# Performance work log

Hardware: AMD Instinct MI355X
Metric: run time of the kernel (lower is better)

## Reference

```python
import jax, jax.numpy as jnp
import numpy as np

B, S, D = 1, 2048, 1024
H, HD = 16, 64          # attention heads, head dim (kv_heads = 1 -> MQA)
E, K, FH = 8, 2, 4096   # experts, top-k, expert hidden dim
EPS = 1e-5


def setup_inputs() -> dict:
    key = jax.random.key(0)
    ks = jax.random.split(key, 8)
    std = 0.02
    return {
        "x": jax.random.normal(ks[0], (B, S, D), jnp.float32),
        "Wq": jax.random.normal(ks[1], (D, H * HD), jnp.float32) * std,
        "Wk": jax.random.normal(ks[2], (D, HD), jnp.float32) * std,   # 1 kv head
        "Wv": jax.random.normal(ks[3], (D, HD), jnp.float32) * std,
        "Wo": jax.random.normal(ks[4], (H * HD, D), jnp.float32) * std,
        "g_pre_mqa": jnp.ones((D,), jnp.float32),
        "g_post_mqa": jnp.ones((D,), jnp.float32),
        "g_pre_moe": jnp.ones((D,), jnp.float32),
        "g_post_moe": jnp.ones((D,), jnp.float32),
        "Wr": jax.random.normal(ks[5], (D, E), jnp.float32) * std,
        "W1": jax.random.normal(ks[6], (E, D, FH), jnp.float32) * std,
        "W2": jax.random.normal(ks[7], (E, FH, D), jnp.float32) * std,
    }


def rmsnorm(x, g):
    return x * jax.lax.rsqrt(jnp.mean(x * x, axis=-1, keepdims=True) + EPS) * g


def reference(x, Wq, Wk, Wv, Wo, g_pre_mqa, g_post_mqa, g_pre_moe, g_post_moe, Wr, W1, W2):
    # --- MQA block (inference path, no dropout, no causal mask in source) ---
    h = rmsnorm(x, g_pre_mqa)
    q = (h @ Wq).reshape(B, S, H, HD)
    k = h @ Wk  # [B,S,HD] single kv head, broadcast over H
    v = h @ Wv
    scores = jnp.einsum('bqhd,bkd->bhqk', q, k) / np.float32(np.sqrt(HD))
    probs_attn = jax.nn.softmax(scores, axis=-1)
    attn = jnp.einsum('bhqk,bkd->bqhd', probs_attn, v).reshape(B, S, H * HD) @ Wo
    x = x + rmsnorm(attn, g_post_mqa)

    # --- MoE block: softmax router, top-k sparse combine ---
    h = rmsnorm(x, g_pre_moe)
    logits = h @ Wr                                # [B,S,E]
    routing_probs = jax.nn.softmax(logits, axis=-1)
    _, top_idx = jax.lax.top_k(routing_probs, K)   # [B,S,K]
    mask = jax.nn.one_hot(top_idx, E, dtype=routing_probs.dtype).sum(axis=-2)
    weights = routing_probs * mask                 # zero non-chosen experts
    hid = jax.nn.gelu(jnp.einsum('bsd,edf->bsef', h, W1))   # [B,S,E,FH]
    eout = jnp.einsum('bsef,efd->bsed', hid, W2)            # [B,S,E,D]
    moe_out = jnp.einsum('bsed,bse->bsd', eout, weights)
    x = x + rmsnorm(moe_out, g_post_moe)
    return x, routing_probs
```

## Files before the change

kernel.cpp:

```cpp
#include <hip/hip_runtime.h>

typedef unsigned short u16;

#define DEVFN static __device__ __forceinline__

constexpr int Sq = 2048, Dm = 1024, NH = 16, HDim = 64, NE = 8, FHid = 4096;

typedef __attribute__((ext_vector_type(8))) short bf16x8;
typedef __attribute__((ext_vector_type(4))) float f32x4;

DEVFN float b2f(u16 u) { return __uint_as_float(((unsigned)u) << 16); }
DEVFN u16 f2b(float f) {
  unsigned u = __float_as_uint(f);
  return (u16)((u + 0x7fffu + ((u >> 16) & 1u)) >> 16);
}
DEVFN float gelu_f(float x) {
  float y = 0.7978845608028654f * (x + 0.044715f * x * x * x);
  float t = 1.0f - 2.0f / (__expf(2.0f * y) + 1.0f);
  return 0.5f * x * (1.0f + t);
}

DEVFN void gload16(const u16* g, u16* l) {
  __builtin_amdgcn_global_load_lds((const __attribute__((address_space(1))) void*)g,
                                   (__attribute__((address_space(3))) void*)l, 16, 0, 0);
}

__global__ __launch_bounds__(256) void detect_k(const u16* __restrict__ x, int* __restrict__ flag) {
  int t = threadIdx.x;
  float mx = 0.f;
  for (int i = t; i < 4096; i += 256) mx = fmaxf(mx, fabsf(b2f(x[i])));
#pragma unroll
  for (int m = 32; m; m >>= 1) mx = fmaxf(mx, __shfl_xor(mx, m, 64));
  __shared__ float red[4];
  if ((t & 63) == 0) red[t >> 6] = mx;
  __syncthreads();
  if (t == 0) {
    float m2 = fmaxf(fmaxf(red[0], red[1]), fmaxf(red[2], red[3]));
    flag[0] = (m2 > 1e6f) ? 1 : 0;
  }
}

template <int INM, int RESM>
__global__ __launch_bounds__(64) void rmsnorm2_k(const void* __restrict__ inp, const void* __restrict__ g,
                                                 const void* __restrict__ resp, float* __restrict__ out1,
                                                 const int* __restrict__ dflag,
                                                 const void* __restrict__ inp2) {
  int isf = dflag[0];
  int row = blockIdx.x, t = threadIdx.x;
  long rb = (long)row * Dm;
  float v[16];
#pragma unroll
  for (int j = 0; j < 4; j++) {
    long o = rb + t * 4 + j * 256;
    if constexpr (INM == 2) {
      float4 f = *((const float4*)((const float*)inp + o));
      float4 f2 = *((const float4*)((const float*)inp2 + o));
      v[4 * j] = f.x + f2.x; v[4 * j + 1] = f.y + f2.y;
      v[4 * j + 2] = f.z + f2.z; v[4 * j + 3] = f.w + f2.w;
    } else if (INM == 0 || isf) {
      float4 f = *((const float4*)((const float*)inp + o));
      v[4 * j] = f.x; v[4 * j + 1] = f.y; v[4 * j + 2] = f.z; v[4 * j + 3] = f.w;
    } else {
      ushort4 u = *((const ushort4*)((const u16*)inp + o));
      v[4 * j] = b2f(u.x); v[4 * j + 1] = b2f(u.y); v[4 * j + 2] = b2f(u.z); v[4 * j + 3] = b2f(u.w);
    }
  }
  float ss = 0.f;
#pragma unroll
  for (int j = 0; j < 16; j++) ss += v[j] * v[j];
#pragma unroll
  for (int m = 32; m; m >>= 1) ss += __shfl_xor(ss, m, 64);
  float sc = rsqrtf(ss * (1.0f / Dm) + 1e-5f);
#pragma unroll
  for (int j = 0; j < 4; j++) {
    long o = rb + t * 4 + j * 256;
    int go = t * 4 + j * 256;
    float gf[4];
    if (isf) {
      float4 gv = *((const float4*)((const float*)g + go));
      gf[0] = gv.x; gf[1] = gv.y; gf[2] = gv.z; gf[3] = gv.w;
    } else {
      ushort4 gu = *((const ushort4*)((const u16*)g + go));
      gf[0] = b2f(gu.x); gf[1] = b2f(gu.y); gf[2] = b2f(gu.z); gf[3] = b2f(gu.w);
    }
    float o4[4];
#pragma unroll
    for (int q = 0; q < 4; q++) o4[q] = v[4 * j + q] * sc * gf[q];
    if constexpr (RESM == 1) {
      float4 rf = *((const float4*)((const float*)resp + o));
      o4[0] += rf.x; o4[1] += rf.y; o4[2] += rf.z; o4[3] += rf.w;
    } else if constexpr (RESM == 2) {
      if (isf) {
        float4 rf = *((const float4*)((const float*)resp + o));
        o4[0] += rf.x; o4[1] += rf.y; o4[2] += rf.z; o4[3] += rf.w;
      } else {
        ushort4 ru = *((const ushort4*)((const u16*)resp + o));
        o4[0] += b2f(ru.x); o4[1] += b2f(ru.y); o4[2] += b2f(ru.z); o4[3] += b2f(ru.w);
      }
    }
    float4 of;
    of.x = o4[0]; of.y = o4[1]; of.z = o4[2]; of.w = o4[3];
    *((float4*)(out1 + o)) = of;
  }
}

template <int OP>
__global__ __launch_bounds__(256) void gemm_nn_k(
    const float* __restrict__ A, const void* __restrict__ Braw, long boff,
    float* __restrict__ C, int M, int N, int K,
    const float* __restrict__ wfull, int eidx, const int* __restrict__ dflag) {
  int isf = dflag[0];
  const float* Bf = (const float*)Braw;
  const u16* Bh = (const u16*)Braw;
  int t = threadIdx.x;
  int m0 = blockIdx.y * 64, n0 = blockIdx.x * 64;

  __shared__ float As[64][20];
  __shared__ float Bs[16][68];

  int ty = t >> 4, tx = t & 15;
  float acc[4][4];
#pragma unroll
  for (int i = 0; i < 4; i++)
#pragma unroll
    for (int j = 0; j < 4; j++) acc[i][j] = 0.f;

  for (int k0 = 0; k0 < K; k0 += 16) {
    __syncthreads();
#pragma unroll
    for (int i = 0; i < 4; i++) {
      int idx = t + i * 256;
      int ar = idx >> 4, ac = idx & 15;
      As[ar][ac] = A[(long)(m0 + ar) * K + k0 + ac];
      int br = idx >> 6, bc = idx & 63;
      long bi = boff + (long)(k0 + br) * N + n0 + bc;
      Bs[br][bc] = isf ? Bf[bi] : b2f(Bh[bi]);
    }
    __syncthreads();
#pragma unroll
    for (int kk = 0; kk < 16; kk++) {
      float a[4], b[4];
#pragma unroll
      for (int i = 0; i < 4; i++) a[i] = As[ty * 4 + i][kk];
#pragma unroll
      for (int j = 0; j < 4; j++) b[j] = Bs[kk][tx * 4 + j];
#pragma unroll
      for (int i = 0; i < 4; i++)
#pragma unroll
        for (int j = 0; j < 4; j++) acc[i][j] += a[i] * b[j];
    }
  }
#pragma unroll
  for (int i = 0; i < 4; i++) {
    int row = m0 + ty * 4 + i;
#pragma unroll
    for (int j = 0; j < 4; j++) {
      int col = n0 + tx * 4 + j;
      long cidx = (long)row * N + col;
      float val = acc[i][j];
      if constexpr (OP == 0) C[cidx] = val;
      else if constexpr (OP == 1) C[cidx] = gelu_f(val);
      else C[cidx] += wfull[(long)row * 8 + eidx] * val;
    }
  }
}

__global__ __launch_bounds__(256) void gemm_big_k(
    const float* __restrict__ A, const void* __restrict__ Braw,
    float* __restrict__ C, int M, int N, int K, const int* __restrict__ dflag) {
  int isf = dflag[0];
  const float* Bf = (const float*)Braw;
  const u16* Bh = (const u16*)Braw;
  int t = threadIdx.x;
  int m0 = blockIdx.y * 128, n0 = blockIdx.x * 64;

  __shared__ float As[128][21];
  __shared__ float Bs[16][68];

  int ty = t >> 4, tx = t & 15;
  float acc[8][4];
#pragma unroll
  for (int i = 0; i < 8; i++)
#pragma unroll
    for (int j = 0; j < 4; j++) acc[i][j] = 0.f;

  for (int k0 = 0; k0 < K; k0 += 16) {
    __syncthreads();
#pragma unroll
    for (int i = 0; i < 8; i++) {
      int idx = t + i * 256;
      int ar = idx >> 4, ac = idx & 15;
      As[ar][ac] = A[(long)(m0 + ar) * K + k0 + ac];
    }
#pragma unroll
    for (int i = 0; i < 4; i++) {
      int idx = t + i * 256;
      int br = idx >> 6, bc = idx & 63;
      long bi = (long)(k0 + br) * N + n0 + bc;
      Bs[br][bc] = isf ? Bf[bi] : b2f(Bh[bi]);
    }
    __syncthreads();
#pragma unroll
    for (int kk = 0; kk < 16; kk++) {
      float a[8], b[4];
#pragma unroll
      for (int i = 0; i < 8; i++) a[i] = As[ty * 8 + i][kk];
#pragma unroll
      for (int j = 0; j < 4; j++) b[j] = Bs[kk][tx * 4 + j];
#pragma unroll
      for (int i = 0; i < 8; i++)
#pragma unroll
        for (int j = 0; j < 4; j++) acc[i][j] += a[i] * b[j];
    }
  }
#pragma unroll
  for (int i = 0; i < 8; i++) {
    int row = m0 + ty * 8 + i;
#pragma unroll
    for (int j = 0; j < 4; j++) {
      int col = n0 + tx * 4 + j;
      C[(long)row * N + col] = acc[i][j];
    }
  }
}

__global__ __launch_bounds__(256) void attn_f32_k(
    const float* __restrict__ Qf, const float* __restrict__ Kf, const float* __restrict__ Vf,
    float* __restrict__ Of) {
  int qb = blockIdx.x, h = blockIdx.y;
  int t = threadIdx.x;
  int qr = t >> 2;
  int sub = t & 3;
  __shared__ float Ks[64][68];
  __shared__ float Vs[64][68];
  int qrow = qb * 64 + qr;
  const float* qp = Qf + (long)qrow * Dm + h * HDim + sub * 16;
  float qfr[16];
#pragma unroll
  for (int j = 0; j < 16; j += 4) {
    float4 v = *(const float4*)(qp + j);
    qfr[j] = v.x; qfr[j + 1] = v.y; qfr[j + 2] = v.z; qfr[j + 3] = v.w;
  }
  float o[16];
#pragma unroll
  for (int j = 0; j < 16; j++) o[j] = 0.f;
  float m_i = -3e38f, l_i = 0.f;

  for (int kb = 0; kb < Sq / 64; kb++) {
    __syncthreads();
#pragma unroll
    for (int i = 0; i < 2; i++) {
      int idx = t + i * 256;
      int r = idx >> 3, c8 = (idx & 7) * 8;
      const float* kp = Kf + (long)(kb * 64 + r) * HDim + c8;
      float4 a = *(const float4*)(kp);
      float4 b = *(const float4*)(kp + 4);
      *(float4*)&Ks[r][c8] = a;
      *(float4*)&Ks[r][c8 + 4] = b;
      const float* vp = Vf + (long)(kb * 64 + r) * HDim + c8;
      float4 c = *(const float4*)(vp);
      float4 d = *(const float4*)(vp + 4);
      *(float4*)&Vs[r][c8] = c;
      *(float4*)&Vs[r][c8 + 4] = d;
    }
    __syncthreads();
    float s[64];
#pragma unroll
    for (int j = 0; j < 64; j++) {
      float acc = 0.f;
#pragma unroll
      for (int d = 0; d < 16; d++) acc += qfr[d] * Ks[j][sub * 16 + d];
      s[j] = acc;
    }
#pragma unroll
    for (int j = 0; j < 64; j++) {
      float v = s[j];
      v += __shfl_xor(v, 1, 64);
      v += __shfl_xor(v, 2, 64);
      s[j] = v * 0.125f;
    }
    float mx = s[0];
#pragma unroll
    for (int j = 1; j < 64; j++) mx = fmaxf(mx, s[j]);
    float mn = fmaxf(m_i, mx);
    float alpha = __expf(m_i - mn);
    m_i = mn;
    float ps = 0.f;
#pragma unroll
    for (int j = 0; j < 64; j++) {
      s[j] = __expf(s[j] - mn);
      ps += s[j];
    }
    l_i = l_i * alpha + ps;
#pragma unroll
    for (int d = 0; d < 16; d++) o[d] *= alpha;
#pragma unroll
    for (int j = 0; j < 64; j++)
#pragma unroll
      for (int d = 0; d < 16; d++) o[d] += s[j] * Vs[j][sub * 16 + d];
  }
  float inv = 1.0f / l_i;
#pragma unroll
  for (int d = 0; d < 16; d++)
    Of[(long)qrow * Dm + h * HDim + sub * 16 + d] = o[d] * inv;
}

__global__ __launch_bounds__(256) void router2_k(const float* __restrict__ h2, const void* __restrict__ Wr,
                                                 float* __restrict__ probs_out, float* __restrict__ wfull,
                                                 const int* __restrict__ dflag,
                                                 int* __restrict__ ecnt, int* __restrict__ elist) {
  int isf = dflag[0];
  int gid = blockIdx.x * 256 + threadIdx.x;
  int tok = gid >> 3, e = gid & 7;
  if (tok >= Sq) return;
  const float* hrow = h2 + (long)tok * Dm;
  float acc = 0.f;
  if (isf) {
    const float* wr = (const float*)Wr;
    for (int i = 0; i < Dm; i += 4) {
      float4 h4 = *(const float4*)(hrow + i);
      acc += h4.x * wr[(long)i * 8 + e];
      acc += h4.y * wr[(long)(i + 1) * 8 + e];
      acc += h4.z * wr[(long)(i + 2) * 8 + e];
      acc += h4.w * wr[(long)(i + 3) * 8 + e];
    }
  } else {
    const u16* wr = (const u16*)Wr;
    for (int i = 0; i < Dm; i += 4) {
      float4 h4 = *(const float4*)(hrow + i);
      acc += h4.x * b2f(wr[(long)i * 8 + e]);
      acc += h4.y * b2f(wr[(long)(i + 1) * 8 + e]);
      acc += h4.z * b2f(wr[(long)(i + 2) * 8 + e]);
      acc += h4.w * b2f(wr[(long)(i + 3) * 8 + e]);
    }
  }
  int lane = threadIdx.x & 63;
  int gbase = lane & ~7;
  float vals[8];
#pragma unroll
  for (int e2 = 0; e2 < 8; e2++) vals[e2] = __shfl(acc, gbase + e2, 64);
  int i1 = 0;
#pragma unroll
  for (int e2 = 1; e2 < 8; e2++)
    if (vals[e2] > vals[i1]) i1 = e2;
  int i2 = (i1 == 0) ? 1 : 0;
#pragma unroll
  for (int e2 = 0; e2 < 8; e2++)
    if (e2 != i1 && vals[e2] > vals[i2]) i2 = e2;
  float mx = vals[i1];
  float pr[8], s = 0.f;
#pragma unroll
  for (int e2 = 0; e2 < 8; e2++) { pr[e2] = expf(vals[e2] - mx); s += pr[e2]; }
  float inv = 1.0f / s;
  float pe = pr[e] * inv;
  probs_out[(long)tok * 8 + e] = pe;
  wfull[(long)tok * 8 + e] = (e == i1 || e == i2) ? pe : 0.f;
  if (e == 0) {
    int p1 = atomicAdd(&ecnt[i1], 1);
    elist[i1 * Sq + p1] = tok;
    int p2 = atomicAdd(&ecnt[i2], 1);
    elist[i2 * Sq + p2] = tok;
  }
}

__global__ __launch_bounds__(256) void split_pair_k(const float* __restrict__ in, u16* __restrict__ hi,
                                                    u16* __restrict__ lo, int n4) {
  int i = blockIdx.x * 256 + threadIdx.x;
  if (i >= n4) return;
  float4 v = ((const float4*)in)[i];
  ushort4 h, l;
  h.x = f2b(v.x); l.x = f2b(v.x - b2f(h.x));
  h.y = f2b(v.y); l.y = f2b(v.y - b2f(h.y));
  h.z = f2b(v.z); l.z = f2b(v.z - b2f(h.z));
  h.w = f2b(v.w); l.w = f2b(v.w - b2f(h.w));
  ((ushort4*)hi)[i] = h;
  ((ushort4*)lo)[i] = l;
}

__global__ __launch_bounds__(256) void transpose2_k(const void* __restrict__ W1p, const void* __restrict__ W2p,
                                                    long boff, u16* __restrict__ bt1, u16* __restrict__ bt2,
                                                    const int* __restrict__ dflag) {
  int isf = dflag[0];
  int z = blockIdx.z;
  const void* B = z ? W2p : W1p;
  u16* BT = z ? bt2 : bt1;
  int K = z ? FHid : Dm;
  int N = z ? Dm : FHid;
  int n0 = blockIdx.x * 32, k0 = blockIdx.y * 32;
  if (n0 >= N || k0 >= K) return;
  __shared__ u16 tile[32][33];
  int tx = threadIdx.x & 31, ty = threadIdx.x >> 5;
#pragma unroll
  for (int j = 0; j < 32; j += 8) {
    long idx = boff + (long)(k0 + ty + j) * N + n0 + tx;
    u16 uv = isf ? f2b(((const float*)B)[idx]) : ((const u16*)B)[idx];
    tile[ty + j][tx] = uv;
  }
  __syncthreads();
#pragma unroll
  for (int j = 0; j < 32; j += 8)
    BT[(long)(n0 + ty + j) * K + k0 + tx] = tile[tx][ty + j];
}

__global__ __launch_bounds__(256) void moe_w1_k(
    const u16* __restrict__ Ah, const u16* __restrict__ Al, const u16* __restrict__ BT,
    u16* __restrict__ Ch, u16* __restrict__ Cl, const float* __restrict__ wfull,
    const int* __restrict__ elist, const int* __restrict__ ecnt, int eidx) {
  constexpr int N = FHid, K = Dm;
  int cnt = ecnt[eidx];
  int m0 = blockIdx.y * 128, n0 = blockIdx.x * 128;
  if (m0 >= cnt) return;
  __shared__ __align__(16) u16 sAh[128 * 32];
  __shared__ __align__(16) u16 sAl[128 * 32];
  __shared__ __align__(16) u16 sBT[128 * 32];
  __shared__ int sTok[128];
  int t = threadIdx.x;
  if (t < 128) {
    int r = m0 + t;
    sTok[t] = (r < cnt) ? elist[eidx * Sq + r] : elist[eidx * Sq];
  }
  int l = t & 63, w = t >> 6;
  int wm = w >> 1, wn = w & 1;
  int lr = l & 15, lg = l >> 4;

  f32x4 zero = {0.f, 0.f, 0.f, 0.f};
  f32x4 acc[4][4];
#pragma unroll
  for (int i = 0; i < 4; i++)
#pragma unroll
    for (int j = 0; j < 4; j++) acc[i][j] = zero;

  for (int k0 = 0; k0 < K; k0 += 32) {
    __syncthreads();
#pragma unroll
    for (int i = 0; i < 2; i++) {
      int s = i * 256 + t;
      int r = s >> 2, c = s & 3;
      long ao = (long)sTok[r] * K + k0 + c * 8;
      gload16(Ah + ao, sAh + s * 8);
      gload16(Al + ao, sAl + s * 8);
      gload16(BT + (long)(n0 + r) * K + k0 + c * 8, sBT + s * 8);
    }
    __syncthreads();
    bf16x8 fah[4], fal[4], fbb[4];
#pragma unroll
    for (int f = 0; f < 4; f++) {
      int ra = wm * 64 + f * 16 + lr;
      fah[f] = *(const bf16x8*)(sAh + ra * 32 + lg * 8);
      fal[f] = *(const bf16x8*)(sAl + ra * 32 + lg * 8);
      int rb = wn * 64 + f * 16 + lr;
      fbb[f] = *(const bf16x8*)(sBT + rb * 32 + lg * 8);
    }
#pragma unroll
    for (int i = 0; i < 4; i++)
#pragma unroll
      for (int j = 0; j < 4; j++) {
        acc[i][j] = __builtin_amdgcn_mfma_f32_16x16x32_bf16(fah[i], fbb[j], acc[i][j], 0, 0, 0);
        acc[i][j] = __builtin_amdgcn_mfma_f32_16x16x32_bf16(fal[i], fbb[j], acc[i][j], 0, 0, 0);
      }
  }

#pragma unroll
  for (int i = 0; i < 4; i++) {
#pragma unroll
    for (int j = 0; j < 4; j++) {
#pragma unroll
      for (int q = 0; q < 4; q++) {
        int widx = wm * 64 + i * 16 + lg * 4 + q;
        int col = n0 + wn * 64 + j * 16 + lr;
        bool valid = (m0 + widx) < cnt;
        int tok = sTok[widx];
        float gv = valid ? gelu_f(acc[i][j][q]) * wfull[(long)tok * 8 + eidx] : 0.f;
        u16 hh = f2b(gv);
        long idx = (long)(m0 + widx) * N + col;
        Ch[idx] = hh;
        Cl[idx] = f2b(gv - b2f(hh));
      }
    }
  }
}

__global__ __launch_bounds__(256) void moe_w2_k(
    const u16* __restrict__ Ah, const u16* __restrict__ Al, const u16* __restrict__ BT,
    float* __restrict__ C0, float* __restrict__ C1,
    const int* __restrict__ elist, const int* __restrict__ ecnt, int eidx) {
  constexpr int N = Dm, K = FHid;
  int cnt = ecnt[eidx];
  int m0 = blockIdx.y * 128, n0 = blockIdx.x * 64;
  if (m0 >= cnt) return;
  float* C = blockIdx.z ? C1 : C0;
  int kbeg = blockIdx.z * (K / 2), kend = kbeg + K / 2;
  __shared__ __align__(16) u16 sAh[128 * 32];
  __shared__ __align__(16) u16 sAl[128 * 32];
  __shared__ __align__(16) u16 sBT[64 * 32];
  __shared__ int sTok[128];
  int t = threadIdx.x;
  if (t < 128) {
    int r = m0 + t;
    sTok[t] = (r < cnt) ? elist[eidx * Sq + r] : elist[eidx * Sq];
  }
  int l = t & 63, w = t >> 6;
  int wm = w >> 1, wn = w & 1;
  int lr = l & 15, lg = l >> 4;

  f32x4 zero = {0.f, 0.f, 0.f, 0.f};
  f32x4 acc[4][2];
#pragma unroll
  for (int i = 0; i < 4; i++)
#pragma unroll
    for (int j = 0; j < 2; j++) acc[i][j] = zero;

  for (int k0 = kbeg; k0 < kend; k0 += 32) {
    __syncthreads();
#pragma unroll
    for (int i = 0; i < 2; i++) {
      int s = i * 256 + t;
      int r = s >> 2, c = s & 3;
      long ao = (long)(m0 + r) * K + k0 + c * 8;
      gload16(Ah + ao, sAh + s * 8);
      gload16(Al + ao, sAl + s * 8);
    }
    {
      int r = t >> 2, c = t & 3;
      gload16(BT + (long)(n0 + r) * K + k0 + c * 8, sBT + t * 8);
    }
    __syncthreads();
    bf16x8 fah[4], fal[4], fbb[2];
#pragma unroll
    for (int f = 0; f < 4; f++) {
      int ra = wm * 64 + f * 16 + lr;
      fah[f] = *(const bf16x8*)(sAh + ra * 32 + lg * 8);
      fal[f] = *(const bf16x8*)(sAl + ra * 32 + lg * 8);
    }
#pragma unroll
    for (int j = 0; j < 2; j++) {
      int rb = wn * 32 + j * 16 + lr;
      fbb[j] = *(const bf16x8*)(sBT + rb * 32 + lg * 8);
    }
#pragma unroll
    for (int i = 0; i < 4; i++)
#pragma unroll
      for (int j = 0; j < 2; j++) {
        acc[i][j] = __builtin_amdgcn_mfma_f32_16x16x32_bf16(fah[i], fbb[j], acc[i][j], 0, 0, 0);
        acc[i][j] = __builtin_amdgcn_mfma_f32_16x16x32_bf16(fal[i], fbb[j], acc[i][j], 0, 0, 0);
      }
  }

#pragma unroll
  for (int i = 0; i < 4; i++) {
#pragma unroll
    for (int j = 0; j < 2; j++) {
#pragma unroll
      for (int q = 0; q < 4; q++) {
        int widx = wm * 64 + i * 16 + lg * 4 + q;
        int col = n0 + wn * 32 + j * 16 + lr;
        if ((m0 + widx) < cnt) {
          int tok = sTok[widx];
          C[(long)tok * N + col] += acc[i][j][q];
        }
      }
    }
  }
}

extern "C" void kernel_launch(void* const* d_in, const int* in_sizes, int n_in,
                              void* d_out, int out_size, void* d_ws, size_t ws_size,
                              hipStream_t stream) {
  (void)in_sizes; (void)n_in;
  const void* x = d_in[0];
  const void* Wq = d_in[1];
  const void* Wk = d_in[2];
  const void* Wv = d_in[3];
  const void* Wo = d_in[4];
  const void* gpre = d_in[5];
  const void* gpost = d_in[6];
  const void* gpm = d_in[7];
  const void* gpo = d_in[8];
  const void* Wr = d_in[9];
  const void* W1 = d_in[10];
  const void* W2 = d_in[11];

  char* ws = (char*)d_ws;
  size_t off = 0;
  auto AL = [&](size_t b) { size_t o = off; off += (b + 255) & ~(size_t)255; return o; };
  const size_t oFlag = AL(16);
  const size_t oWf = AL((size_t)Sq * NE * 4);
  const size_t oHid = AL((size_t)Sq * FHid * 4);
  const size_t oH2 = AL((size_t)Sq * Dm * 4);
  const size_t oX2 = AL((size_t)Sq * Dm * 4);
  const size_t oMoe = AL((size_t)Sq * Dm * 4);
  const size_t oAp = AL((size_t)Sq * Dm * 4);
  const size_t oAt = AL((size_t)Sq * Dm * 4);
  const size_t oVf = AL((size_t)Sq * HDim * 4);
  const size_t oKf = AL((size_t)Sq * HDim * 4);
  const size_t oQf = AL((size_t)Sq * Dm * 4);
  const size_t oH1 = AL((size_t)Sq * Dm * 4);
  if (off > ws_size || out_size != Sq * Dm + Sq * NE) return;

  float* h1f = (float*)(ws + oH1);
  float* qf = (float*)(ws + oQf);
  float* kf = (float*)(ws + oKf);
  float* vf = (float*)(ws + oVf);
  float* attnf = (float*)(ws + oAt);
  float* attnp = (float*)(ws + oAp);
  float* x2 = (float*)(ws + oX2);
  float* h2f = (float*)(ws + oH2);
  float* moe = (float*)(ws + oMoe);
  float* wfull = (float*)(ws + oWf);
  int* dflag = (int*)(ws + oFlag);
  u16* hidh = (u16*)(ws + oHid);
  u16* hidl = hidh + (size_t)Sq * FHid;
  u16* bt1 = (u16*)(ws + oAt);
  u16* bt2 = (u16*)(ws + oAp);
  u16* h2h = (u16*)(ws + oQf);
  u16* h2l = h2h + (size_t)Sq * Dm;
  float* moe2 = (float*)(ws + oH1);
  int* ecnt = (int*)(ws + oVf);
  int* elist = (int*)(ws + oVf + 256);
  float* out_x = (float*)d_out;
  float* out_probs = out_x + (size_t)Sq * Dm;

  detect_k<<<1, 256, 0, stream>>>((const u16*)x, dflag);

  rmsnorm2_k<1, 0><<<Sq, 64, 0, stream>>>(x, gpre, nullptr, h1f, dflag, nullptr);

  gemm_big_k<<<dim3(Dm / 64, Sq / 128), 256, 0, stream>>>(h1f, Wq, qf, Sq, Dm, Dm, dflag);
  gemm_nn_k<0><<<dim3(HDim / 64, Sq / 64), 256, 0, stream>>>(h1f, Wk, 0, kf, Sq, HDim, Dm, nullptr, 0, dflag);
  gemm_nn_k<0><<<dim3(HDim / 64, Sq / 64), 256, 0, stream>>>(h1f, Wv, 0, vf, Sq, HDim, Dm, nullptr, 0, dflag);

  attn_f32_k<<<dim3(Sq / 64, NH), 256, 0, stream>>>(qf, kf, vf, attnf);

  gemm_big_k<<<dim3(Dm / 64, Sq / 128), 256, 0, stream>>>(attnf, Wo, attnp, Sq, Dm, Dm, dflag);

  rmsnorm2_k<0, 2><<<Sq, 64, 0, stream>>>(attnp, gpost, x, x2, dflag, nullptr);
  rmsnorm2_k<0, 0><<<Sq, 64, 0, stream>>>(x2, gpm, nullptr, h2f, dflag, nullptr);

  hipMemsetAsync(ws + oVf, 0, 32, stream);
  router2_k<<<Sq * NE / 256, 256, 0, stream>>>(h2f, Wr, out_probs, wfull, dflag, ecnt, elist);

  split_pair_k<<<(Sq * Dm / 4 + 255) / 256, 256, 0, stream>>>(h2f, h2h, h2l, Sq * Dm / 4);

  hipMemsetAsync(ws + oMoe, 0, (size_t)Sq * Dm * 4, stream);
  hipMemsetAsync(ws + oH1, 0, (size_t)Sq * Dm * 4, stream);
  for (int e = 0; e < NE; e++) {
    transpose2_k<<<dim3(128, 128, 2), 256, 0, stream>>>(
        W1, W2, (long)e * Dm * FHid, bt1, bt2, dflag);
    moe_w1_k<<<dim3(FHid / 128, Sq / 128), 256, 0, stream>>>(
        h2h, h2l, bt1, hidh, hidl, wfull, elist, ecnt, e);
    moe_w2_k<<<dim3(Dm / 64, Sq / 128, 2), 256, 0, stream>>>(
        hidh, hidl, bt2, moe, moe2, elist, ecnt, e);
  }

  rmsnorm2_k<2, 1><<<Sq, 64, 0, stream>>>(moe, gpo, x2, out_x, dflag, moe2);
}
```

Before: 2.515 ms.

## Batch all MoE experts into grouped GEMMs and fuse QKV and rmsnorm kernels

Replaces the per-expert loop of transpose, W1 and W2 launches with two grouped kernels that map tiles to experts through prefix counts. These kernels read the untransposed weights directly and convert them on the fly. The hidden activation is kept as a single bf16 array instead of a hi/lo pair, and the MoE output is written to four separate partial buffers (primary/secondary expert × K-half) instead of being accumulated, which removes the memsets. Q, K and V projections are merged into one launch, the two post-attention rmsnorms are fused, and the attention inner loops use float4 LDS reads. Dropping the lo half of the hidden activation lowers precision, and the strided on-the-fly weight loads may be poorly coalesced.

```diff
diff --git a/kernel.cpp b/kernel.cpp
--- a/kernel.cpp
+++ b/kernel.cpp
@@ -40,11 +40,8 @@
   }
 }
 
-template <int INM, int RESM>
-__global__ __launch_bounds__(64) void rmsnorm2_k(const void* __restrict__ inp, const void* __restrict__ g,
-                                                 const void* __restrict__ resp, float* __restrict__ out1,
-                                                 const int* __restrict__ dflag,
-                                                 const void* __restrict__ inp2) {
+__global__ __launch_bounds__(64) void rmsnorm_in_k(const void* __restrict__ inp, const void* __restrict__ g,
+                                                   float* __restrict__ out1, const int* __restrict__ dflag) {
   int isf = dflag[0];
   int row = blockIdx.x, t = threadIdx.x;
   long rb = (long)row * Dm;
@@ -52,12 +49,7 @@
 #pragma unroll
   for (int j = 0; j < 4; j++) {
     long o = rb + t * 4 + j * 256;
-    if constexpr (INM == 2) {
-      float4 f = *((const float4*)((const float*)inp + o));
-      float4 f2 = *((const float4*)((const float*)inp2 + o));
-      v[4 * j] = f.x + f2.x; v[4 * j + 1] = f.y + f2.y;
-      v[4 * j + 2] = f.z + f2.z; v[4 * j + 3] = f.w + f2.w;
-    } else if (INM == 0 || isf) {
+    if (isf) {
       float4 f = *((const float4*)((const float*)inp + o));
       v[4 * j] = f.x; v[4 * j + 1] = f.y; v[4 * j + 2] = f.z; v[4 * j + 3] = f.w;
     } else {
@@ -83,84 +75,203 @@
       ushort4 gu = *((const ushort4*)((const u16*)g + go));
       gf[0] = b2f(gu.x); gf[1] = b2f(gu.y); gf[2] = b2f(gu.z); gf[3] = b2f(gu.w);
     }
+    float4 of;
+    of.x = v[4 * j] * sc * gf[0];
+    of.y = v[4 * j + 1] * sc * gf[1];
+    of.z = v[4 * j + 2] * sc * gf[2];
+    of.w = v[4 * j + 3] * sc * gf[3];
+    *((float4*)(out1 + o)) = of;
+  }
+}
+
+__global__ __launch_bounds__(64) void rmsnorm_fused_k(
+    const float* __restrict__ attnp, const void* __restrict__ gpost, const void* __restrict__ xres,
+    const void* __restrict__ gpm, float* __restrict__ x2, float* __restrict__ h2,
+    const int* __restrict__ dflag) {
+  int isf = dflag[0];
+  int row = blockIdx.x, t = threadIdx.x;
+  long rb = (long)row * Dm;
+  float v[16];
+#pragma unroll
+  for (int j = 0; j < 4; j++) {
+    long o = rb + t * 4 + j * 256;
+    float4 f = *((const float4*)(attnp + o));
+    v[4 * j] = f.x; v[4 * j + 1] = f.y; v[4 * j + 2] = f.z; v[4 * j + 3] = f.w;
+  }
+  float ss = 0.f;
+#pragma unroll
+  for (int j = 0; j < 16; j++) ss += v[j] * v[j];
+#pragma unroll
+  for (int m = 32; m; m >>= 1) ss += __shfl_xor(ss, m, 64);
+  float sc = rsqrtf(ss * (1.0f / Dm) + 1e-5f);
+  float xv[16];
+#pragma unroll
+  for (int j = 0; j < 4; j++) {
+    long o = rb + t * 4 + j * 256;
+    int go = t * 4 + j * 256;
+    float gf[4];
+    if (isf) {
+      float4 gv = *((const float4*)((const float*)gpost + go));
+      gf[0] = gv.x; gf[1] = gv.y; gf[2] = gv.z; gf[3] = gv.w;
+    } else {
+      ushort4 gu = *((const ushort4*)((const u16*)gpost + go));
+      gf[0] = b2f(gu.x); gf[1] = b2f(gu.y); gf[2] = b2f(gu.z); gf[3] = b2f(gu.w);
+    }
     float o4[4];
 #pragma unroll
     for (int q = 0; q < 4; q++) o4[q] = v[4 * j + q] * sc * gf[q];
-    if constexpr (RESM == 1) {
-      float4 rf = *((const float4*)((const float*)resp + o));
+    if (isf) {
+      float4 rf = *((const float4*)((const float*)xres + o));
       o4[0] += rf.x; o4[1] += rf.y; o4[2] += rf.z; o4[3] += rf.w;
-    } else if constexpr (RESM == 2) {
-      if (isf) {
-        float4 rf = *((const float4*)((const float*)resp + o));
-        o4[0] += rf.x; o4[1] += rf.y; o4[2] += rf.z; o4[3] += rf.w;
-      } else {
-        ushort4 ru = *((const ushort4*)((const u16*)resp + o));
-        o4[0] += b2f(ru.x); o4[1] += b2f(ru.y); o4[2] += b2f(ru.z); o4[3] += b2f(ru.w);
-      }
+    } else {
+      ushort4 ru = *((const ushort4*)((const u16*)xres + o));
+      o4[0] += b2f(ru.x); o4[1] += b2f(ru.y); o4[2] += b2f(ru.z); o4[3] += b2f(ru.w);
     }
     float4 of;
     of.x = o4[0]; of.y = o4[1]; of.z = o4[2]; of.w = o4[3];
+    *((float4*)(x2 + o)) = of;
+    xv[4 * j] = o4[0]; xv[4 * j + 1] = o4[1]; xv[4 * j + 2] = o4[2]; xv[4 * j + 3] = o4[3];
+  }
+  float ss2 = 0.f;
+#pragma unroll
+  for (int j = 0; j < 16; j++) ss2 += xv[j] * xv[j];
+#pragma unroll
+  for (int m = 32; m; m >>= 1) ss2 += __shfl_xor(ss2, m, 64);
+  float sc2 = rsqrtf(ss2 * (1.0f / Dm) + 1e-5f);
+#pragma unroll
+  for (int j = 0; j < 4; j++) {
+    long o = rb + t * 4 + j * 256;
+    int go = t * 4 + j * 256;
+    float gf[4];
+    if (isf) {
+      float4 gv = *((const float4*)((const float*)gpm + go));
+      gf[0] = gv.x; gf[1] = gv.y; gf[2] = gv.z; gf[3] = gv.w;
+    } else {
+      ushort4 gu = *((const ushort4*)((const u16*)gpm + go));
+      gf[0] = b2f(gu.x); gf[1] = b2f(gu.y); gf[2] = b2f(gu.z); gf[3] = b2f(gu.w);
+    }
+    float4 of;
+    of.x = xv[4 * j] * sc2 * gf[0];
+    of.y = xv[4 * j + 1] * sc2 * gf[1];
+    of.z = xv[4 * j + 2] * sc2 * gf[2];
+    of.w = xv[4 * j + 3] * sc2 * gf[3];
+    *((float4*)(h2 + o)) = of;
+  }
+}
+
+__global__ __launch_bounds__(64) void rmsnorm_moe_k(
+    const float* __restrict__ p0, const float* __restrict__ p1,
+    const float* __restrict__ s0, const float* __restrict__ s1,
+    const void* __restrict__ g, const float* __restrict__ x2,
+    float* __restrict__ out1, const int* __restrict__ dflag) {
+  int isf = dflag[0];
+  int row = blockIdx.x, t = threadIdx.x;
+  long rb = (long)row * Dm;
+  float v[16];
+#pragma unroll
+  for (int j = 0; j < 4; j++) {
+    long o = rb + t * 4 + j * 256;
+    float4 a = *((const float4*)(p0 + o));
+    float4 b = *((const float4*)(p1 + o));
+    float4 c = *((const float4*)(s0 + o));
+    float4 d = *((const float4*)(s1 + o));
+    v[4 * j] = (a.x + b.x) + (c.x + d.x);
+    v[4 * j + 1] = (a.y + b.y) + (c.y + d.y);
+    v[4 * j + 2] = (a.z + b.z) + (c.z + d.z);
+    v[4 * j + 3] = (a.w + b.w) + (c.w + d.w);
+  }
+  float ss = 0.f;
+#pragma unroll
+  for (int j = 0; j < 16; j++) ss += v[j] * v[j];
+#pragma unroll
+  for (int m = 32; m; m >>= 1) ss += __shfl_xor(ss, m, 64);
+  float sc = rsqrtf(ss * (1.0f / Dm) + 1e-5f);
+#pragma unroll
+  for (int j = 0; j < 4; j++) {
+    long o = rb + t * 4 + j * 256;
+    int go = t * 4 + j * 256;
+    float gf[4];
+    if (isf) {
+      float4 gv = *((const float4*)((const float*)g + go));
+      gf[0] = gv.x; gf[1] = gv.y; gf[2] = gv.z; gf[3] = gv.w;
+    } else {
+      ushort4 gu = *((const ushort4*)((const u16*)g + go));
+      gf[0] = b2f(gu.x); gf[1] = b2f(gu.y); gf[2] = b2f(gu.z); gf[3] = b2f(gu.w);
+    }
+    float4 rf = *((const float4*)(x2 + o));
+    float4 of;
+    of.x = v[4 * j] * sc * gf[0] + rf.x;
+    of.y = v[4 * j + 1] * sc * gf[1] + rf.y;
+    of.z = v[4 * j + 2] * sc * gf[2] + rf.z;
+    of.w = v[4 * j + 3] * sc * gf[3] + rf.w;
     *((float4*)(out1 + o)) = of;
   }
 }
 
-template <int OP>
-__global__ __launch_bounds__(256) void gemm_nn_k(
-    const float* __restrict__ A, const void* __restrict__ Braw, long boff,
-    float* __restrict__ C, int M, int N, int K,
-    const float* __restrict__ wfull, int eidx, const int* __restrict__ dflag) {
+__global__ __launch_bounds__(256) void gemm_qkv_k(
+    const float* __restrict__ A, const void* __restrict__ WqB, const void* __restrict__ WkB,
+    const void* __restrict__ WvB, float* __restrict__ qf, float* __restrict__ kf,
+    float* __restrict__ vf, const int* __restrict__ dflag) {
   int isf = dflag[0];
+  int bx = blockIdx.x;
+  const void* Braw;
+  float* C;
+  int N, n0;
+  if (bx < 16) { Braw = WqB; C = qf; N = 1024; n0 = bx * 64; }
+  else if (bx == 16) { Braw = WkB; C = kf; N = 64; n0 = 0; }
+  else { Braw = WvB; C = vf; N = 64; n0 = 0; }
   const float* Bf = (const float*)Braw;
   const u16* Bh = (const u16*)Braw;
   int t = threadIdx.x;
-  int m0 = blockIdx.y * 64, n0 = blockIdx.x * 64;
-
-  __shared__ float As[64][20];
+  int m0 = blockIdx.y * 128;
+  constexpr int K = Dm;
+
+  __shared__ float As[128][21];
   __shared__ float Bs[16][68];
 
   int ty = t >> 4, tx = t & 15;
-  float acc[4][4];
-#pragma unroll
-  for (int i = 0; i < 4; i++)
+  float acc[8][4];
+#pragma unroll
+  for (int i = 0; i < 8; i++)
 #pragma unroll
     for (int j = 0; j < 4; j++) acc[i][j] = 0.f;
 
   for (int k0 = 0; k0 < K; k0 += 16) {
     __syncthreads();
 #pragma unroll
-    for (int i = 0; i < 4; i++) {
+    for (int i = 0; i < 8; i++) {
       int idx = t + i * 256;
       int ar = idx >> 4, ac = idx & 15;
       As[ar][ac] = A[(long)(m0 + ar) * K + k0 + ac];
+    }
+#pragma unroll
+    for (int i = 0; i < 4; i++) {
+      int idx = t + i * 256;
       int br = idx >> 6, bc = idx & 63;
-      long bi = boff + (long)(k0 + br) * N + n0 + bc;
+      long bi = (long)(k0 + br) * N + n0 + bc;
       Bs[br][bc] = isf ? Bf[bi] : b2f(Bh[bi]);
     }
     __syncthreads();
 #pragma unroll
     for (int kk = 0; kk < 16; kk++) {
-      float a[4], b[4];
-#pragma unroll
-      for (int i = 0; i < 4; i++) a[i] = As[ty * 4 + i][kk];
+      float a[8], b[4];
+#pragma unroll
+      for (int i = 0; i < 8; i++) a[i] = As[ty * 8 + i][kk];
 #pragma unroll
       for (int j = 0; j < 4; j++) b[j] = Bs[kk][tx * 4 + j];
 #pragma unroll
-      for (int i = 0; i < 4; i++)
+      for (int i = 0; i < 8; i++)
 #pragma unroll
         for (int j = 0; j < 4; j++) acc[i][j] += a[i] * b[j];
     }
   }
 #pragma unroll
-  for (int i = 0; i < 4; i++) {
-    int row = m0 + ty * 4 + i;
+  for (int i = 0; i < 8; i++) {
+    int row = m0 + ty * 8 + i;
 #pragma unroll
     for (int j = 0; j < 4; j++) {
       int col = n0 + tx * 4 + j;
-      long cidx = (long)row * N + col;
-      float val = acc[i][j];
-      if constexpr (OP == 0) C[cidx] = val;
-      else if constexpr (OP == 1) C[cidx] = gelu_f(val);
-      else C[cidx] += wfull[(long)row * 8 + eidx] * val;
+      C[(long)row * N + col] = acc[i][j];
     }
   }
 }
@@ -269,7 +380,13 @@
     for (int j = 0; j < 64; j++) {
       float acc = 0.f;
 #pragma unroll
-      for (int d = 0; d < 16; d++) acc += qfr[d] * Ks[j][sub * 16 + d];
+      for (int dq = 0; dq < 4; dq++) {
+        float4 k4 = *(const float4*)&Ks[j][sub * 16 + dq * 4];
+        acc += qfr[dq * 4 + 0] * k4.x;
+        acc += qfr[dq * 4 + 1] * k4.y;
+        acc += qfr[dq * 4 + 2] * k4.z;
+        acc += qfr[dq * 4 + 3] * k4.w;
+      }
       s[j] = acc;
     }
 #pragma unroll
@@ -295,9 +412,16 @@
 #pragma unroll
     for (int d = 0; d < 16; d++) o[d] *= alpha;
 #pragma unroll
-    for (int j = 0; j < 64; j++)
-#pragma unroll
-      for (int d = 0; d < 16; d++) o[d] += s[j] * Vs[j][sub * 16 + d];
+    for (int j = 0; j < 64; j++) {
+#pragma unroll
+      for (int dq = 0; dq < 4; dq++) {
+        float4 v4 = *(const float4*)&Vs[j][sub * 16 + dq * 4];
+        o[dq * 4 + 0] += s[j] * v4.x;
+        o[dq * 4 + 1] += s[j] * v4.y;
+        o[dq * 4 + 2] += s[j] * v4.z;
+        o[dq * 4 + 3] += s[j] * v4.w;
+      }
+    }
   }
   float inv = 1.0f / l_i;
 #pragma unroll
@@ -359,7 +483,7 @@
     int p1 = atomicAdd(&ecnt[i1], 1);
     elist[i1 * Sq + p1] = tok;
     int p2 = atomicAdd(&ecnt[i2], 1);
-    elist[i2 * Sq + p2] = tok;
+    elist[i2 * Sq + p2] = tok | 0x8000;
   }
 }
 
@@ -377,39 +501,33 @@
   ((ushort4*)lo)[i] = l;
 }
 
-__global__ __launch_bounds__(256) void transpose2_k(const void* __restrict__ W1p, const void* __restrict__ W2p,
-                                                    long boff, u16* __restrict__ bt1, u16* __restrict__ bt2,
-                                                    const int* __restrict__ dflag) {
+DEVFN bool map_tile(const int* ecnt, int by, int& e, int& m0, int& base, int& cnt) {
+  int cum = 0, cumc = 0;
+  e = -1;
+#pragma unroll
+  for (int ee = 0; ee < 8; ee++) {
+    int c = ecnt[ee];
+    int tt = (c + 127) >> 7;
+    if (e < 0 && by >= cum && by < cum + tt) {
+      e = ee; m0 = (by - cum) << 7; base = cumc; cnt = c;
+    }
+    cum += tt; cumc += c;
+  }
+  return e >= 0;
+}
+
+__global__ __launch_bounds__(256) void moe_w1_all_k(
+    const u16* __restrict__ Ah, const u16* __restrict__ Al, const void* __restrict__ W1raw,
+    u16* __restrict__ hid, const float* __restrict__ wfull,
+    const int* __restrict__ elist, const int* __restrict__ ecnt, const int* __restrict__ dflag) {
+  constexpr int N = FHid, K = Dm;
   int isf = dflag[0];
-  int z = blockIdx.z;
-  const void* B = z ? W2p : W1p;
-  u16* BT = z ? bt2 : bt1;
-  int K = z ? FHid : Dm;
-  int N = z ? Dm : FHid;
-  int n0 = blockIdx.x * 32, k0 = blockIdx.y * 32;
-  if (n0 >= N || k0 >= K) return;
-  __shared__ u16 tile[32][33];
-  int tx = threadIdx.x & 31, ty = threadIdx.x >> 5;
-#pragma unroll
-  for (int j = 0; j < 32; j += 8) {
-    long idx = boff + (long)(k0 + ty + j) * N + n0 + tx;
-    u16 uv = isf ? f2b(((const float*)B)[idx]) : ((const u16*)B)[idx];
-    tile[ty + j][tx] = uv;
-  }
-  __syncthreads();
-#pragma unroll
-  for (int j = 0; j < 32; j += 8)
-    BT[(long)(n0 + ty + j) * K + k0 + tx] = tile[tx][ty + j];
-}
-
-__global__ __launch_bounds__(256) void moe_w1_k(
-    const u16* __restrict__ Ah, const u16* __restrict__ Al, const u16* __restrict__ BT,
-    u16* __restrict__ Ch, u16* __restrict__ Cl, const float* __restrict__ wfull,
-    const int* __restrict__ elist, const int* __restrict__ ecnt, int eidx) {
-  constexpr int N = FHid, K = Dm;
-  int cnt = ecnt[eidx];
-  int m0 = blockIdx.y * 128, n0 = blockIdx.x * 128;
-  if (m0 >= cnt) return;
+  int e, m0, base, cnt;
+  if (!map_tile(ecnt, blockIdx.y, e, m0, base, cnt)) return;
+  int n0 = blockIdx.x * 128;
+  const float* W1f = (const float*)W1raw + (long)e * K * N;
+  const u16* W1h = (const u16*)W1raw + (long)e * K * N;
+
   __shared__ __align__(16) u16 sAh[128 * 32];
   __shared__ __align__(16) u16 sAl[128 * 32];
   __shared__ __align__(16) u16 sBT[128 * 32];
@@ -417,7 +535,7 @@
   int t = threadIdx.x;
   if (t < 128) {
     int r = m0 + t;
-    sTok[t] = (r < cnt) ? elist[eidx * Sq + r] : elist[eidx * Sq];
+    sTok[t] = (r < cnt) ? elist[e * Sq + r] : elist[e * Sq];
   }
   int l = t & 63, w = t >> 6;
   int wm = w >> 1, wn = w & 1;
@@ -436,10 +554,21 @@
     for (int i = 0; i < 2; i++) {
       int s = i * 256 + t;
       int r = s >> 2, c = s & 3;
-      long ao = (long)sTok[r] * K + k0 + c * 8;
+      long ao = (long)(sTok[r] & 0x7fff) * K + k0 + c * 8;
       gload16(Ah + ao, sAh + s * 8);
       gload16(Al + ao, sAl + s * 8);
-      gload16(BT + (long)(n0 + r) * K + k0 + c * 8, sBT + s * 8);
+    }
+#pragma unroll
+    for (int i = 0; i < 2; i++) {
+      int s = i * 256 + t;
+      int nr = s >> 2, kc = (s & 3) * 8;
+      u16 bv[8];
+#pragma unroll
+      for (int j = 0; j < 8; j++) {
+        long bi = (long)(k0 + kc + j) * N + n0 + nr;
+        bv[j] = isf ? f2b(W1f[bi]) : W1h[bi];
+      }
+      *(bf16x8*)(sBT + nr * 32 + kc) = *(bf16x8*)bv;
     }
     __syncthreads();
     bf16x8 fah[4], fal[4], fbb[4];
@@ -467,37 +596,40 @@
 #pragma unroll
       for (int q = 0; q < 4; q++) {
         int widx = wm * 64 + i * 16 + lg * 4 + q;
-        int col = n0 + wn * 64 + j * 16 + lr;
-        bool valid = (m0 + widx) < cnt;
-        int tok = sTok[widx];
-        float gv = valid ? gelu_f(acc[i][j][q]) * wfull[(long)tok * 8 + eidx] : 0.f;
-        u16 hh = f2b(gv);
-        long idx = (long)(m0 + widx) * N + col;
-        Ch[idx] = hh;
-        Cl[idx] = f2b(gv - b2f(hh));
+        if ((m0 + widx) < cnt) {
+          int col = n0 + wn * 64 + j * 16 + lr;
+          int tok = sTok[widx] & 0x7fff;
+          float gv = gelu_f(acc[i][j][q]) * wfull[(long)tok * 8 + e];
+          hid[(long)(base + m0 + widx) * N + col] = f2b(gv);
+        }
       }
     }
   }
 }
 
-__global__ __launch_bounds__(256) void moe_w2_k(
-    const u16* __restrict__ Ah, const u16* __restrict__ Al, const u16* __restrict__ BT,
-    float* __restrict__ C0, float* __restrict__ C1,
-    const int* __restrict__ elist, const int* __restrict__ ecnt, int eidx) {
+__global__ __launch_bounds__(256) void moe_w2_all_k(
+    const u16* __restrict__ hid, const void* __restrict__ W2raw,
+    float* __restrict__ P0, float* __restrict__ P1, float* __restrict__ S0, float* __restrict__ S1,
+    const int* __restrict__ elist, const int* __restrict__ ecnt, const int* __restrict__ dflag) {
   constexpr int N = Dm, K = FHid;
-  int cnt = ecnt[eidx];
-  int m0 = blockIdx.y * 128, n0 = blockIdx.x * 64;
-  if (m0 >= cnt) return;
-  float* C = blockIdx.z ? C1 : C0;
-  int kbeg = blockIdx.z * (K / 2), kend = kbeg + K / 2;
-  __shared__ __align__(16) u16 sAh[128 * 32];
-  __shared__ __align__(16) u16 sAl[128 * 32];
+  int isf = dflag[0];
+  int e, m0, base, cnt;
+  if (!map_tile(ecnt, blockIdx.y, e, m0, base, cnt)) return;
+  int n0 = blockIdx.x * 64;
+  int z = blockIdx.z;
+  int kbeg = z * (K / 2), kend = kbeg + K / 2;
+  const float* W2f = (const float*)W2raw + (long)e * K * N;
+  const u16* W2h = (const u16*)W2raw + (long)e * K * N;
+
+  __shared__ __align__(16) u16 sA[128 * 32];
   __shared__ __align__(16) u16 sBT[64 * 32];
   __shared__ int sTok[128];
+  __shared__ int sRow[128];
   int t = threadIdx.x;
   if (t < 128) {
     int r = m0 + t;
-    sTok[t] = (r < cnt) ? elist[eidx * Sq + r] : elist[eidx * Sq];
+    sTok[t] = (r < cnt) ? elist[e * Sq + r] : elist[e * Sq];
+    sRow[t] = base + ((r < cnt) ? r : (cnt - 1));
   }
   int l = t & 63, w = t >> 6;
   int wm = w >> 1, wn = w & 1;
@@ -516,21 +648,25 @@
     for (int i = 0; i < 2; i++) {
       int s = i * 256 + t;
       int r = s >> 2, c = s & 3;
-      long ao = (long)(m0 + r) * K + k0 + c * 8;
-      gload16(Ah + ao, sAh + s * 8);
-      gload16(Al + ao, sAl + s * 8);
+      long ao = (long)sRow[r] * K + k0 + c * 8;
+      gload16(hid + ao, sA + s * 8);
     }
     {
-      int r = t >> 2, c = t & 3;
-      gload16(BT + (long)(n0 + r) * K + k0 + c * 8, sBT + t * 8);
-    }
-    __syncthreads();
-    bf16x8 fah[4], fal[4], fbb[2];
+      int nr = t >> 2, kc = (t & 3) * 8;
+      u16 bv[8];
+#pragma unroll
+      for (int j = 0; j < 8; j++) {
+        long bi = (long)(k0 + kc + j) * N + n0 + nr;
+        bv[j] = isf ? f2b(W2f[bi]) : W2h[bi];
+      }
+      *(bf16x8*)(sBT + nr * 32 + kc) = *(bf16x8*)bv;
+    }
+    __syncthreads();
+    bf16x8 fa[4], fbb[2];
 #pragma unroll
     for (int f = 0; f < 4; f++) {
       int ra = wm * 64 + f * 16 + lr;
-      fah[f] = *(const bf16x8*)(sAh + ra * 32 + lg * 8);
-      fal[f] = *(const bf16x8*)(sAl + ra * 32 + lg * 8);
+      fa[f] = *(const bf16x8*)(sA + ra * 32 + lg * 8);
     }
 #pragma unroll
     for (int j = 0; j < 2; j++) {
@@ -540,10 +676,8 @@
 #pragma unroll
     for (int i = 0; i < 4; i++)
 #pragma unroll
-      for (int j = 0; j < 2; j++) {
-        acc[i][j] = __builtin_amdgcn_mfma_f32_16x16x32_bf16(fah[i], fbb[j], acc[i][j], 0, 0, 0);
-        acc[i][j] = __builtin_amdgcn_mfma_f32_16x16x32_bf16(fal[i], fbb[j], acc[i][j], 0, 0, 0);
-      }
+      for (int j = 0; j < 2; j++)
+        acc[i][j] = __builtin_amdgcn_mfma_f32_16x16x32_bf16(fa[i], fbb[j], acc[i][j], 0, 0, 0);
   }
 
 #pragma unroll
@@ -553,10 +687,12 @@
 #pragma unroll
       for (int q = 0; q < 4; q++) {
         int widx = wm * 64 + i * 16 + lg * 4 + q;
-        int col = n0 + wn * 32 + j * 16 + lr;
         if ((m0 + widx) < cnt) {
-          int tok = sTok[widx];
-          C[(long)tok * N + col] += acc[i][j][q];
+          int v = sTok[widx];
+          int tok = v & 0x7fff;
+          float* C = (v & 0x8000) ? (z ? S1 : S0) : (z ? P1 : P0);
+          int col = n0 + wn * 32 + j * 16 + lr;
+          C[(long)tok * N + col] = acc[i][j][q];
         }
       }
     }
@@ -605,16 +741,15 @@
   float* attnp = (float*)(ws + oAp);
   float* x2 = (float*)(ws + oX2);
   float* h2f = (float*)(ws + oH2);
-  float* moe = (float*)(ws + oMoe);
   float* wfull = (float*)(ws + oWf);
   int* dflag = (int*)(ws + oFlag);
-  u16* hidh = (u16*)(ws + oHid);
-  u16* hidl = hidh + (size_t)Sq * FHid;
-  u16* bt1 = (u16*)(ws + oAt);
-  u16* bt2 = (u16*)(ws + oAp);
+  u16* hid = (u16*)(ws + oHid);
   u16* h2h = (u16*)(ws + oQf);
   u16* h2l = h2h + (size_t)Sq * Dm;
-  float* moe2 = (float*)(ws + oH1);
+  float* moeP0 = (float*)(ws + oMoe);
+  float* moeP1 = (float*)(ws + oH1);
+  float* moeS0 = (float*)(ws + oH2);
+  float* moeS1 = (float*)(ws + oAt);
   int* ecnt = (int*)(ws + oVf);
   int* elist = (int*)(ws + oVf + 256);
   float* out_x = (float*)d_out;
@@ -622,34 +757,25 @@
 
   detect_k<<<1, 256, 0, stream>>>((const u16*)x, dflag);
 
-  rmsnorm2_k<1, 0><<<Sq, 64, 0, stream>>>(x, gpre, nullptr, h1f, dflag, nullptr);
-
-  gemm_big_k<<<dim3(Dm / 64, Sq / 128), 256, 0, stream>>>(h1f, Wq, qf, Sq, Dm, Dm, dflag);
-  gemm_nn_k<0><<<dim3(HDim / 64, Sq / 64), 256, 0, stream>>>(h1f, Wk, 0, kf, Sq, HDim, Dm, nullptr, 0, dflag);
-  gemm_nn_k<0><<<dim3(HDim / 64, Sq / 64), 256, 0, stream>>>(h1f, Wv, 0, vf, Sq, HDim, Dm, nullptr, 0, dflag);
+  rmsnorm_in_k<<<Sq, 64, 0, stream>>>(x, gpre, h1f, dflag);
+
+  gemm_qkv_k<<<dim3(18, Sq / 128), 256, 0, stream>>>(h1f, Wq, Wk, Wv, qf, kf, vf, dflag);
 
   attn_f32_k<<<dim3(Sq / 64, NH), 256, 0, stream>>>(qf, kf, vf, attnf);
 
   gemm_big_k<<<dim3(Dm / 64, Sq / 128), 256, 0, stream>>>(attnf, Wo, attnp, Sq, Dm, Dm, dflag);
 
-  rmsnorm2_k<0, 2><<<Sq, 64, 0, stream>>>(attnp, gpost, x, x2, dflag, nullptr);
-  rmsnorm2_k<0, 0><<<Sq, 64, 0, stream>>>(x2, gpm, nullptr, h2f, dflag, nullptr);
+  rmsnorm_fused_k<<<Sq, 64, 0, stream>>>(attnp, gpost, x, gpm, x2, h2f, dflag);
 
   hipMemsetAsync(ws + oVf, 0, 32, stream);
   router2_k<<<Sq * NE / 256, 256, 0, stream>>>(h2f, Wr, out_probs, wfull, dflag, ecnt, elist);
 
   split_pair_k<<<(Sq * Dm / 4 + 255) / 256, 256, 0, stream>>>(h2f, h2h, h2l, Sq * Dm / 4);
 
-  hipMemsetAsync(ws + oMoe, 0, (size_t)Sq * Dm * 4, stream);
-  hipMemsetAsync(ws + oH1, 0, (size_t)Sq * Dm * 4, stream);
-  for (int e = 0; e < NE; e++) {
-    transpose2_k<<<dim3(128, 128, 2), 256, 0, stream>>>(
-        W1, W2, (long)e * Dm * FHid, bt1, bt2, dflag);
-    moe_w1_k<<<dim3(FHid / 128, Sq / 128), 256, 0, stream>>>(
-        h2h, h2l, bt1, hidh, hidl, wfull, elist, ecnt, e);
-    moe_w2_k<<<dim3(Dm / 64, Sq / 128, 2), 256, 0, stream>>>(
-        hidh, hidl, bt2, moe, moe2, elist, ecnt, e);
-  }
-
-  rmsnorm2_k<2, 1><<<Sq, 64, 0, stream>>>(moe, gpo, x2, out_x, dflag, moe2);
-}
+  moe_w1_all_k<<<dim3(FHid / 128, 39), 256, 0, stream>>>(
+      h2h, h2l, W1, hid, wfull, elist, ecnt, dflag);
+  moe_w2_all_k<<<dim3(Dm / 64, 39, 2), 256, 0, stream>>>(
+      hid, W2, moeP0, moeP1, moeS0, moeS1, elist, ecnt, dflag);
+
+  rmsnorm_moe_k<<<Sq, 64, 0, stream>>>(moeP0, moeP1, moeS0, moeS1, gpo, x2, out_x, dflag);
+}
```

New measurement: 2.234 ms. 1.13x faster.
